# Kernel optimization log

Hardware: AMD Instinct MI355X
Metric: run time of the kernel (lower is better)

Reference implementation:

```python
import jax, jax.numpy as jnp
import numpy as np

B = 4096   # batch_size from init_kwargs
D = 128    # embedding dim
TEMP = 0.25


def _l2_normalize(x, eps=1e-12):
    # matches F.normalize(dim=1): x / max(||x||, eps)
    n = jnp.linalg.norm(x, axis=1, keepdims=True)
    return x / jnp.maximum(n, eps)


def setup_inputs() -> dict:
    key = jax.random.key(0)
    k1, k2 = jax.random.split(key)
    return {
        "emb_i": jax.random.normal(k1, (B, D), dtype=jnp.float32),
        "emb_j": jax.random.normal(k2, (B, D), dtype=jnp.float32),
    }


def reference(emb_i, emb_j):
    b = emb_i.shape[0]
    z_i = _l2_normalize(emb_i)
    z_j = _l2_normalize(emb_j)
    reps = jnp.concatenate([z_i, z_j], axis=0)            # [2B, D]
    # cosine similarity of normalized vectors == dot product
    sim = reps @ reps.T                                    # [2B, 2B]
    sim_ij = jnp.diagonal(sim, offset=b)                   # [B]
    sim_ji = jnp.diagonal(sim, offset=-b)                  # [B]
    positives = jnp.concatenate([sim_ij, sim_ji], axis=0)  # [2B]
    # negatives_mask as overwritten in __init__: ones only on the two
    # off-diagonal cross-view blocks.
    mask = (
        jnp.zeros((2 * b, 2 * b), dtype=sim.dtype)
        .at[:b, b:].set(1.0)
        .at[b:, :b].set(1.0)
    )
    exp_sim = jnp.exp(sim / TEMP)                          # [2B, 2B]
    denom = jnp.sum(mask * exp_sim, axis=1)                # [2B]
    loss_partial = -jnp.log(jnp.exp(positives / TEMP) / denom)
    loss = jnp.sum(loss_partial) / (2 * b)
    return loss
```

## Files before the change

### kernel.cpp

```cpp
#include <hip/hip_runtime.h>

#define BATCH 4096
#define DIM   128
#define TILE  256
#define NT    16
#define EXP_SCALE 5.770780163555854f

typedef __bf16 bf16_t;
typedef __bf16 bf16x4 __attribute__((ext_vector_type(4)));
typedef __bf16 bf16x8 __attribute__((ext_vector_type(8)));
typedef float  f32x4  __attribute__((ext_vector_type(4)));

__global__ __launch_bounds__(512, 2) void fused_kernel(
    const float* __restrict__ emb_i, const float* __restrict__ emb_j,
    float* __restrict__ rowP,
    float* __restrict__ colP,
    float* __restrict__ pos, float* __restrict__ out)
{
    __shared__ __align__(16) bf16_t zi_s[TILE][136];
    __shared__ __align__(16) bf16_t zj_s[TILE][136];
    __shared__ float rowRed[4][TILE];
    __shared__ float colRed[2][TILE];

    const int tid = threadIdx.x;
    const int ti = blockIdx.x, tj = blockIdx.y;

    if ((ti | tj) == 0 && tid == 0) out[0] = 0.0f;

    {
        const int g  = tid >> 5;
        const int gl = tid & 31;
        const float* bi = emb_i + (size_t)ti * TILE * DIM;
        const float* bj = emb_j + (size_t)tj * TILE * DIM;
#pragma unroll
        for (int it = 0; it < 16; ++it) {
            const int r = it * 16 + g;
            float4 a = *(const float4*)(bi + r * DIM + gl * 4);
            float4 b = *(const float4*)(bj + r * DIM + gl * 4);
            float sii = a.x * a.x + a.y * a.y + a.z * a.z + a.w * a.w;
            float sjj = b.x * b.x + b.y * b.y + b.z * b.z + b.w * b.w;
            float sij = a.x * b.x + a.y * b.y + a.z * b.z + a.w * b.w;
#pragma unroll
            for (int m = 1; m < 32; m <<= 1) {
                sii += __shfl_xor(sii, m);
                sjj += __shfl_xor(sjj, m);
                sij += __shfl_xor(sij, m);
            }
            const float inv_i = 1.0f / fmaxf(sqrtf(sii), 1e-12f);
            const float inv_j = 1.0f / fmaxf(sqrtf(sjj), 1e-12f);
            bf16x4 pi, pj;
            pi[0] = (bf16_t)(a.x * inv_i); pi[1] = (bf16_t)(a.y * inv_i);
            pi[2] = (bf16_t)(a.z * inv_i); pi[3] = (bf16_t)(a.w * inv_i);
            pj[0] = (bf16_t)(b.x * inv_j); pj[1] = (bf16_t)(b.y * inv_j);
            pj[2] = (bf16_t)(b.z * inv_j); pj[3] = (bf16_t)(b.w * inv_j);
            *(bf16x4*)&zi_s[r][gl * 4] = pi;
            *(bf16x4*)&zj_s[r][gl * 4] = pj;
            if (ti == tj && gl == 0) pos[ti * TILE + r] = sij * inv_i * inv_j;
        }
    }
    __syncthreads();

    const int wave = tid >> 6;
    const int lane = tid & 63;
    const int l15  = lane & 15;
    const int quad = lane >> 4;
    const int wr   = wave >> 2;
    const int wc   = wave & 3;

    f32x4 acc[8][4];
#pragma unroll
    for (int mr = 0; mr < 8; ++mr)
#pragma unroll
        for (int nc = 0; nc < 4; ++nc)
            acc[mr][nc] = (f32x4){0.f, 0.f, 0.f, 0.f};

#pragma unroll
    for (int ks = 0; ks < 4; ++ks) {
        const int k0 = ks * 32 + quad * 8;
        bf16x8 afrag[8], bfrag[4];
#pragma unroll
        for (int mr = 0; mr < 8; ++mr)
            afrag[mr] = *(const bf16x8*)&zi_s[wr * 128 + mr * 16 + l15][k0];
#pragma unroll
        for (int nc = 0; nc < 4; ++nc)
            bfrag[nc] = *(const bf16x8*)&zj_s[wc * 64 + nc * 16 + l15][k0];
#pragma unroll
        for (int mr = 0; mr < 8; ++mr)
#pragma unroll
            for (int nc = 0; nc < 4; ++nc)
                acc[mr][nc] = __builtin_amdgcn_mfma_f32_16x16x32_bf16(
                    afrag[mr], bfrag[nc], acc[mr][nc], 0, 0, 0);
    }

    float rowPart[8][4];
    float colPart[4] = {0.f, 0.f, 0.f, 0.f};
#pragma unroll
    for (int mr = 0; mr < 8; ++mr)
#pragma unroll
        for (int rr = 0; rr < 4; ++rr) rowPart[mr][rr] = 0.f;

#pragma unroll
    for (int mr = 0; mr < 8; ++mr)
#pragma unroll
        for (int nc = 0; nc < 4; ++nc)
#pragma unroll
            for (int rr = 0; rr < 4; ++rr) {
                const float e = exp2f(acc[mr][nc][rr] * EXP_SCALE);
                rowPart[mr][rr] += e;
                colPart[nc]     += e;
            }

#pragma unroll
    for (int mr = 0; mr < 8; ++mr)
#pragma unroll
        for (int rr = 0; rr < 4; ++rr) {
            float v = rowPart[mr][rr];
            v += __shfl_xor(v, 1);
            v += __shfl_xor(v, 2);
            v += __shfl_xor(v, 4);
            v += __shfl_xor(v, 8);
            if (l15 == 0)
                rowRed[wc][wr * 128 + mr * 16 + quad * 4 + rr] = v;
        }
#pragma unroll
    for (int nc = 0; nc < 4; ++nc) {
        float v = colPart[nc];
        v += __shfl_xor(v, 16);
        v += __shfl_xor(v, 32);
        if (quad == 0)
            colRed[wr][wc * 64 + nc * 16 + l15] = v;
    }
    __syncthreads();

    if (tid < TILE) {
        const float v = rowRed[0][tid] + rowRed[1][tid] +
                        rowRed[2][tid] + rowRed[3][tid];
        rowP[(size_t)tj * BATCH + ti * TILE + tid] = v;
    } else if (tid < 2 * TILE) {
        const int c = tid - TILE;
        colP[(size_t)ti * BATCH + tj * TILE + c] = colRed[0][c] + colRed[1][c];
    }
}

__global__ __launch_bounds__(256) void finalize_kernel(
    const float* __restrict__ rowP, const float* __restrict__ colP,
    const float* __restrict__ pos, float* __restrict__ out)
{
    const int k = blockIdx.x * 256 + threadIdx.x;
    float rd = 0.f, cd = 0.f;
#pragma unroll
    for (int t = 0; t < NT; ++t) {
        rd += rowP[t * BATCH + k];
        cd += colP[t * BATCH + k];
    }
    float v = logf(rd) + logf(cd) - 8.0f * pos[k];
#pragma unroll
    for (int m = 1; m < 64; m <<= 1) v += __shfl_xor(v, m);
    __shared__ float red[4];
    if ((threadIdx.x & 63) == 0) red[threadIdx.x >> 6] = v;
    __syncthreads();
    if (threadIdx.x == 0)
        atomicAdd(out, (red[0] + red[1] + red[2] + red[3]) *
                           (1.0f / (2.0f * BATCH)));
}

extern "C" void kernel_launch(void* const* d_in, const int* in_sizes, int n_in,
                              void* d_out, int out_size, void* d_ws, size_t ws_size,
                              hipStream_t stream) {
    const float* emb_i = (const float*)d_in[0];
    const float* emb_j = (const float*)d_in[1];
    float* out = (float*)d_out;

    char* ws = (char*)d_ws;
    float* rowP = (float*)ws;
    float* colP = (float*)(ws + NT * BATCH * 4);
    float* pos  = (float*)(ws + 2 * (NT * BATCH * 4));

    fused_kernel<<<dim3(NT, NT), 512, 0, stream>>>(emb_i, emb_j, rowP, colP,
                                                   pos, out);
    finalize_kernel<<<BATCH / 256, 256, 0, stream>>>(rowP, colP, pos, out);
}
```

Measured before the change: 81.04 us.

## Split normalization into separate kernel and shrink GEMM tiles to 128

Moves L2 normalization and bf16 conversion out of the fused GEMM kernel into a standalone pass that writes normalized bf16 rows to workspace. The previous version normalized every row NT times, once per tile pair. The GEMM+exp kernel now loads pre-normalized bf16 tiles and uses 128x128 tiles with 256 threads, giving a 32x32 grid for better occupancy across CUs. The cost is an extra launch, a bf16 global round trip, and twice as many partial sums for finalize to reduce.

```diff
diff --git a/kernel.cpp b/kernel.cpp
--- a/kernel.cpp
+++ b/kernel.cpp
@@ -2,61 +2,73 @@
 
 #define BATCH 4096
 #define DIM   128
-#define TILE  256
-#define NT    16
+#define NT    32
 #define EXP_SCALE 5.770780163555854f
 
 typedef __bf16 bf16_t;
-typedef __bf16 bf16x4 __attribute__((ext_vector_type(4)));
 typedef __bf16 bf16x8 __attribute__((ext_vector_type(8)));
 typedef float  f32x4  __attribute__((ext_vector_type(4)));
 
-__global__ __launch_bounds__(512, 2) void fused_kernel(
+__global__ __launch_bounds__(256) void normalize_kernel(
     const float* __restrict__ emb_i, const float* __restrict__ emb_j,
+    bf16_t* __restrict__ zi, bf16_t* __restrict__ zj, float* __restrict__ pos,
+    float* __restrict__ out)
+{
+    if (blockIdx.x == 0 && threadIdx.x == 0) out[0] = 0.0f;
+
+    const int wave = threadIdx.x >> 6;
+    const int lane = threadIdx.x & 63;
+    const int k = blockIdx.x * 4 + wave;
+
+    const float2* ei = (const float2*)(emb_i + (size_t)k * DIM);
+    const float2* ej = (const float2*)(emb_j + (size_t)k * DIM);
+    float2 a = ei[lane];
+    float2 b = ej[lane];
+
+    float sii = a.x * a.x + a.y * a.y;
+    float sjj = b.x * b.x + b.y * b.y;
+    float sij = a.x * b.x + a.y * b.y;
+#pragma unroll
+    for (int m = 1; m < 64; m <<= 1) {
+        sii += __shfl_xor(sii, m);
+        sjj += __shfl_xor(sjj, m);
+        sij += __shfl_xor(sij, m);
+    }
+    const float inv_i = 1.0f / fmaxf(sqrtf(sii), 1e-12f);
+    const float inv_j = 1.0f / fmaxf(sqrtf(sjj), 1e-12f);
+
+    struct bf16_2 { bf16_t x, y; };
+    bf16_2 pi, pj;
+    pi.x = (bf16_t)(a.x * inv_i);  pi.y = (bf16_t)(a.y * inv_i);
+    pj.x = (bf16_t)(b.x * inv_j);  pj.y = (bf16_t)(b.y * inv_j);
+    ((bf16_2*)(zi + (size_t)k * DIM))[lane] = pi;
+    ((bf16_2*)(zj + (size_t)k * DIM))[lane] = pj;
+
+    if (lane == 0) pos[k] = sij * inv_i * inv_j;
+}
+
+__global__ __launch_bounds__(256, 2) void gemm_exp_kernel(
+    const bf16_t* __restrict__ zi, const bf16_t* __restrict__ zj,
     float* __restrict__ rowP,
-    float* __restrict__ colP,
-    float* __restrict__ pos, float* __restrict__ out)
+    float* __restrict__ colP)
 {
-    __shared__ __align__(16) bf16_t zi_s[TILE][136];
-    __shared__ __align__(16) bf16_t zj_s[TILE][136];
-    __shared__ float rowRed[4][TILE];
-    __shared__ float colRed[2][TILE];
+    __shared__ __align__(16) bf16_t zi_s[128][136];
+    __shared__ __align__(16) bf16_t zj_s[128][136];
+    __shared__ float rowRed[2][128];
+    __shared__ float colRed[2][128];
 
     const int tid = threadIdx.x;
     const int ti = blockIdx.x, tj = blockIdx.y;
 
-    if ((ti | tj) == 0 && tid == 0) out[0] = 0.0f;
-
-    {
-        const int g  = tid >> 5;
-        const int gl = tid & 31;
-        const float* bi = emb_i + (size_t)ti * TILE * DIM;
-        const float* bj = emb_j + (size_t)tj * TILE * DIM;
 #pragma unroll
-        for (int it = 0; it < 16; ++it) {
-            const int r = it * 16 + g;
-            float4 a = *(const float4*)(bi + r * DIM + gl * 4);
-            float4 b = *(const float4*)(bj + r * DIM + gl * 4);
-            float sii = a.x * a.x + a.y * a.y + a.z * a.z + a.w * a.w;
-            float sjj = b.x * b.x + b.y * b.y + b.z * b.z + b.w * b.w;
-            float sij = a.x * b.x + a.y * b.y + a.z * b.z + a.w * b.w;
-#pragma unroll
-            for (int m = 1; m < 32; m <<= 1) {
-                sii += __shfl_xor(sii, m);
-                sjj += __shfl_xor(sjj, m);
-                sij += __shfl_xor(sij, m);
-            }
-            const float inv_i = 1.0f / fmaxf(sqrtf(sii), 1e-12f);
-            const float inv_j = 1.0f / fmaxf(sqrtf(sjj), 1e-12f);
-            bf16x4 pi, pj;
-            pi[0] = (bf16_t)(a.x * inv_i); pi[1] = (bf16_t)(a.y * inv_i);
-            pi[2] = (bf16_t)(a.z * inv_i); pi[3] = (bf16_t)(a.w * inv_i);
-            pj[0] = (bf16_t)(b.x * inv_j); pj[1] = (bf16_t)(b.y * inv_j);
-            pj[2] = (bf16_t)(b.z * inv_j); pj[3] = (bf16_t)(b.w * inv_j);
-            *(bf16x4*)&zi_s[r][gl * 4] = pi;
-            *(bf16x4*)&zj_s[r][gl * 4] = pj;
-            if (ti == tj && gl == 0) pos[ti * TILE + r] = sij * inv_i * inv_j;
-        }
+    for (int it = 0; it < 8; ++it) {
+        int c = it * 256 + tid;
+        int row = c >> 4;
+        int col = (c & 15) << 3;
+        *(uint4*)&zi_s[row][col] =
+            *(const uint4*)(zi + ((size_t)(ti * 128 + row)) * DIM + col);
+        *(uint4*)&zj_s[row][col] =
+            *(const uint4*)(zj + ((size_t)(tj * 128 + row)) * DIM + col);
     }
     __syncthreads();
 
@@ -64,12 +76,12 @@
     const int lane = tid & 63;
     const int l15  = lane & 15;
     const int quad = lane >> 4;
-    const int wr   = wave >> 2;
-    const int wc   = wave & 3;
+    const int wr   = wave >> 1;
+    const int wc   = wave & 1;
 
-    f32x4 acc[8][4];
+    f32x4 acc[4][4];
 #pragma unroll
-    for (int mr = 0; mr < 8; ++mr)
+    for (int mr = 0; mr < 4; ++mr)
 #pragma unroll
         for (int nc = 0; nc < 4; ++nc)
             acc[mr][nc] = (f32x4){0.f, 0.f, 0.f, 0.f};
@@ -77,30 +89,30 @@
 #pragma unroll
     for (int ks = 0; ks < 4; ++ks) {
         const int k0 = ks * 32 + quad * 8;
-        bf16x8 afrag[8], bfrag[4];
+        bf16x8 afrag[4], bfrag[4];
 #pragma unroll
-        for (int mr = 0; mr < 8; ++mr)
-            afrag[mr] = *(const bf16x8*)&zi_s[wr * 128 + mr * 16 + l15][k0];
+        for (int mr = 0; mr < 4; ++mr)
+            afrag[mr] = *(const bf16x8*)&zi_s[wr * 64 + mr * 16 + l15][k0];
 #pragma unroll
         for (int nc = 0; nc < 4; ++nc)
             bfrag[nc] = *(const bf16x8*)&zj_s[wc * 64 + nc * 16 + l15][k0];
 #pragma unroll
-        for (int mr = 0; mr < 8; ++mr)
+        for (int mr = 0; mr < 4; ++mr)
 #pragma unroll
             for (int nc = 0; nc < 4; ++nc)
                 acc[mr][nc] = __builtin_amdgcn_mfma_f32_16x16x32_bf16(
                     afrag[mr], bfrag[nc], acc[mr][nc], 0, 0, 0);
     }
 
-    float rowPart[8][4];
+    float rowPart[4][4];
     float colPart[4] = {0.f, 0.f, 0.f, 0.f};
 #pragma unroll
-    for (int mr = 0; mr < 8; ++mr)
+    for (int mr = 0; mr < 4; ++mr)
 #pragma unroll
         for (int rr = 0; rr < 4; ++rr) rowPart[mr][rr] = 0.f;
 
 #pragma unroll
-    for (int mr = 0; mr < 8; ++mr)
+    for (int mr = 0; mr < 4; ++mr)
 #pragma unroll
         for (int nc = 0; nc < 4; ++nc)
 #pragma unroll
@@ -111,7 +123,7 @@
             }
 
 #pragma unroll
-    for (int mr = 0; mr < 8; ++mr)
+    for (int mr = 0; mr < 4; ++mr)
 #pragma unroll
         for (int rr = 0; rr < 4; ++rr) {
             float v = rowPart[mr][rr];
@@ -120,7 +132,7 @@
             v += __shfl_xor(v, 4);
             v += __shfl_xor(v, 8);
             if (l15 == 0)
-                rowRed[wc][wr * 128 + mr * 16 + quad * 4 + rr] = v;
+                rowRed[wc][wr * 64 + mr * 16 + quad * 4 + rr] = v;
         }
 #pragma unroll
     for (int nc = 0; nc < 4; ++nc) {
@@ -132,13 +144,13 @@
     }
     __syncthreads();
 
-    if (tid < TILE) {
-        const float v = rowRed[0][tid] + rowRed[1][tid] +
-                        rowRed[2][tid] + rowRed[3][tid];
-        rowP[(size_t)tj * BATCH + ti * TILE + tid] = v;
-    } else if (tid < 2 * TILE) {
-        const int c = tid - TILE;
-        colP[(size_t)ti * BATCH + tj * TILE + c] = colRed[0][c] + colRed[1][c];
+    if (tid < 128) {
+        rowP[(size_t)tj * BATCH + ti * 128 + tid] =
+            rowRed[0][tid] + rowRed[1][tid];
+    } else if (tid < 256) {
+        const int c = tid - 128;
+        colP[(size_t)ti * BATCH + tj * 128 + c] =
+            colRed[0][c] + colRed[1][c];
     }
 }
 
@@ -150,8 +162,8 @@
     float rd = 0.f, cd = 0.f;
 #pragma unroll
     for (int t = 0; t < NT; ++t) {
-        rd += rowP[t * BATCH + k];
-        cd += colP[t * BATCH + k];
+        rd += rowP[(size_t)t * BATCH + k];
+        cd += colP[(size_t)t * BATCH + k];
     }
     float v = logf(rd) + logf(cd) - 8.0f * pos[k];
 #pragma unroll
@@ -172,11 +184,13 @@
     float* out = (float*)d_out;
 
     char* ws = (char*)d_ws;
-    float* rowP = (float*)ws;
-    float* colP = (float*)(ws + NT * BATCH * 4);
-    float* pos  = (float*)(ws + 2 * (NT * BATCH * 4));
+    bf16_t* zi   = (bf16_t*)(ws);
+    bf16_t* zj   = (bf16_t*)(ws + (1u << 20));
+    float*  rowP = (float*)(ws + (2u << 20));
+    float*  colP = (float*)(ws + (2u << 20) + (512u << 10));
+    float*  pos  = (float*)(ws + (3u << 20));
 
-    fused_kernel<<<dim3(NT, NT), 512, 0, stream>>>(emb_i, emb_j, rowP, colP,
-                                                   pos, out);
+    normalize_kernel<<<BATCH / 4, 256, 0, stream>>>(emb_i, emb_j, zi, zj, pos, out);
+    gemm_exp_kernel<<<dim3(NT, NT), 256, 0, stream>>>(zi, zj, rowP, colP);
     finalize_kernel<<<BATCH / 256, 256, 0, stream>>>(rowP, colP, pos, out);
 }
```

After: 94.43 us. 16.5% more time.
